# Optimization experiments

Hardware: AMD Instinct MI355X
Metric: run time of the kernel (lower is better)

## Reference

```python
import jax, jax.numpy as jnp
import numpy as np

NHEAD = 8
K_NEIGH = 16


def setup_inputs() -> dict:
    key = jax.random.key(0)
    ks = jax.random.split(key, 6)
    B, L, D = 4, 4096, 512
    x = jax.random.normal(ks[0], (B, L, D), dtype=jnp.float32)
    positions = jax.random.uniform(ks[1], (B, L, 3), dtype=jnp.float32)
    in_proj_w = jax.random.normal(ks[2], (3 * D, D), dtype=jnp.float32) * 0.02
    in_proj_b = jax.random.normal(ks[3], (3 * D,), dtype=jnp.float32) * 0.02
    out_proj_w = jax.random.normal(ks[4], (D, D), dtype=jnp.float32) * 0.02
    out_proj_b = jax.random.normal(ks[5], (D,), dtype=jnp.float32) * 0.02
    return {"x": x, "positions": positions, "in_proj_w": in_proj_w,
            "in_proj_b": in_proj_b, "out_proj_w": out_proj_w, "out_proj_b": out_proj_b}


def _sparse_attention(x, positions, in_proj_w, in_proj_b, out_proj_w, out_proj_b):
    B, L, D = x.shape
    H, dh = NHEAD, D // NHEAD
    K = min(K_NEIGH, L)
    scale = 1.0 / jnp.sqrt(jnp.asarray(dh, x.dtype))

    # Pairwise distances [B, L, L]; topk smallest -> neighbor indices [B, L, K].
    diff = positions[:, :, None, :] - positions[:, None, :, :]
    dist = jnp.sqrt(jnp.sum(diff * diff, axis=-1))
    _, nbr = jax.lax.top_k(-dist, K)  # [B, L, K]

    Wq, Wk, Wv = in_proj_w[:D], in_proj_w[D:2 * D], in_proj_w[2 * D:]
    bq, bk, bv = in_proj_b[:D], in_proj_b[D:2 * D], in_proj_b[2 * D:]

    # Query is x[b, i] itself (self is always its own nearest neighbor at dist 0),
    # so the selected attention row equals attention with query x[b, i] over neighbors.
    q = ((x @ Wq.T + bq) * scale).reshape(B, L, H, dh)

    # Gather neighbor features: [B, L, K, D]
    b_idx = jnp.arange(B)[:, None, None]
    local_x = x[b_idx, nbr]
    k = (local_x @ Wk.T + bk).reshape(B, L, K, H, dh)
    v = (local_x @ Wv.T + bv).reshape(B, L, K, H, dh)

    scores = jnp.einsum('blhd,blkhd->blhk', q, k)
    attn = jax.nn.softmax(scores, axis=-1)
    ctx = jnp.einsum('blhk,blkhd->blhd', attn, v).reshape(B, L, D)
    out = ctx @ out_proj_w.T + out_proj_b

    # Faithful fallback: if i not among its neighbors, pass through x[b, i].
    is_in = jnp.any(nbr == jnp.arange(L)[None, :, None], axis=-1)  # [B, L]
    return jnp.where(is_in[..., None], out, x)


def reference(x, positions, in_proj_w, in_proj_b, out_proj_w, out_proj_b):
    return _sparse_attention(x, positions, in_proj_w, in_proj_b, out_proj_w, out_proj_b)
```

## Files before the change

kernel.cpp:

```cpp
#include <hip/hip_runtime.h>
#include <cfloat>
#include <cmath>

constexpr int B = 4;
constexpr int L = 4096;
constexpr int D = 512;
constexpr int NH = 8;
constexpr int DH = 64;
constexpr int KN = 16;
constexpr int M = B * L;
constexpr int N_IN = 3 * D;
constexpr int NCELL = 512;

typedef __attribute__((ext_vector_type(8))) short short8;
typedef __attribute__((ext_vector_type(4))) float f32x4;
typedef unsigned short ushort;

__device__ __forceinline__ ushort f2bf(float f) {
  unsigned u = __float_as_uint(f);
  u = u + 0x7fffu + ((u >> 16) & 1u);
  return (ushort)(u >> 16);
}
__device__ __forceinline__ float bf2f(ushort h) {
  return __uint_as_float(((unsigned)h) << 16);
}
__device__ __forceinline__ float dot8(const uint4 qu, const uint4 ku, float a) {
  a = fmaf(bf2f((ushort)qu.x), bf2f((ushort)ku.x), a);
  a = fmaf(bf2f((ushort)(qu.x >> 16)), bf2f((ushort)(ku.x >> 16)), a);
  a = fmaf(bf2f((ushort)qu.y), bf2f((ushort)ku.y), a);
  a = fmaf(bf2f((ushort)(qu.y >> 16)), bf2f((ushort)(ku.y >> 16)), a);
  a = fmaf(bf2f((ushort)qu.z), bf2f((ushort)ku.z), a);
  a = fmaf(bf2f((ushort)(qu.z >> 16)), bf2f((ushort)(ku.z >> 16)), a);
  a = fmaf(bf2f((ushort)qu.w), bf2f((ushort)ku.w), a);
  a = fmaf(bf2f((ushort)(qu.w >> 16)), bf2f((ushort)(ku.w >> 16)), a);
  return a;
}
__device__ __forceinline__ void acc8(float wgt, const uint4 vv, float (&acc)[8]) {
  acc[0] = fmaf(wgt, bf2f((ushort)vv.x), acc[0]);
  acc[1] = fmaf(wgt, bf2f((ushort)(vv.x >> 16)), acc[1]);
  acc[2] = fmaf(wgt, bf2f((ushort)vv.y), acc[2]);
  acc[3] = fmaf(wgt, bf2f((ushort)(vv.y >> 16)), acc[3]);
  acc[4] = fmaf(wgt, bf2f((ushort)vv.z), acc[4]);
  acc[5] = fmaf(wgt, bf2f((ushort)(vv.z >> 16)), acc[5]);
  acc[6] = fmaf(wgt, bf2f((ushort)vv.w), acc[6]);
  acc[7] = fmaf(wgt, bf2f((ushort)(vv.w >> 16)), acc[7]);
}
__device__ __forceinline__ uint2 pack4hi(const float4 v) {
  uint2 o;
  o.x = (unsigned)f2bf(v.x) | ((unsigned)f2bf(v.y) << 16);
  o.y = (unsigned)f2bf(v.z) | ((unsigned)f2bf(v.w) << 16);
  return o;
}
__device__ __forceinline__ void gload16(const void* g, void* l) {
  __builtin_amdgcn_global_load_lds(
      (const __attribute__((address_space(1))) void*)g,
      (__attribute__((address_space(3))) void*)l, 16, 0, 0);
}
__device__ __forceinline__ int morton3(int x, int y, int z) {
  int m = 0;
#pragma unroll
  for (int i = 0; i < 3; ++i)
    m |= (((x >> i) & 1) << (3 * i + 2)) | (((y >> i) & 1) << (3 * i + 1)) |
         (((z >> i) & 1) << (3 * i));
  return m;
}

constexpr int SORT_BLKS = B;
constexpr int CVTX_BLKS = 1024;
constexpr int CVTW_BLKS = 256;
constexpr int STAGE0_BLKS = SORT_BLKS + CVTX_BLKS + CVTW_BLKS;

__global__ __launch_bounds__(512) void stage0_kernel(
    const float* __restrict__ pos, const float* __restrict__ x,
    const float* __restrict__ in_w, const float* __restrict__ out_w,
    int* __restrict__ qorder, ushort* __restrict__ xb,
    ushort* __restrict__ iwh, ushort* __restrict__ owh,
    ushort* __restrict__ owl) {
  __shared__ int hist[NCELL];
  __shared__ int scanbuf[NCELL];

  const int bid = blockIdx.x;
  const int tid = threadIdx.x;

  if (bid < SORT_BLKS) {
    const int b = bid;
    const int t = tid;
    hist[t] = 0;
    __syncthreads();

    int cells[8], ranks[8];
    const float* p = pos + (size_t)b * L * 3;
#pragma unroll
    for (int q = 0; q < 8; ++q) {
      const int i = q * 512 + t;
      const int ix = min(7, max(0, (int)(p[3 * i + 0] * 8.f)));
      const int iy = min(7, max(0, (int)(p[3 * i + 1] * 8.f)));
      const int iz = min(7, max(0, (int)(p[3 * i + 2] * 8.f)));
      cells[q] = morton3(ix, iy, iz);
      ranks[q] = atomicAdd(&hist[cells[q]], 1);
    }
    __syncthreads();

    int accv = hist[t];
    const int orig = accv;
    scanbuf[t] = accv;
    __syncthreads();
    for (int s = 1; s < NCELL; s <<= 1) {
      const int o = (t >= s) ? scanbuf[t - s] : 0;
      __syncthreads();
      accv += o;
      scanbuf[t] = accv;
      __syncthreads();
    }
    hist[t] = accv - orig;
    __syncthreads();

#pragma unroll
    for (int q = 0; q < 8; ++q) {
      const int i = q * 512 + t;
      qorder[b * L + hist[cells[q]] + ranks[q]] = i;
    }

  } else if (bid < SORT_BLKS + CVTX_BLKS) {
    const int vb = bid - SORT_BLKS;
    const int n8 = M * D / 8;
    for (int i = vb * 512 + tid; i < n8; i += CVTX_BLKS * 512) {
      const float4 v0 = reinterpret_cast<const float4*>(x)[i * 2];
      const float4 v1 = reinterpret_cast<const float4*>(x)[i * 2 + 1];
      uint4 o;
      const uint2 a = pack4hi(v0), b2 = pack4hi(v1);
      o.x = a.x; o.y = a.y; o.z = b2.x; o.w = b2.y;
      reinterpret_cast<uint4*>(xb)[i] = o;
    }

  } else {
    const int vb = bid - SORT_BLKS - CVTX_BLKS;
    const int ni8 = N_IN * D / 8;
    const int no8 = D * D / 8;
    for (int i = vb * 512 + tid; i < ni8 + no8; i += CVTW_BLKS * 512) {
      if (i < ni8) {
        const float4 v0 = reinterpret_cast<const float4*>(in_w)[i * 2];
        const float4 v1 = reinterpret_cast<const float4*>(in_w)[i * 2 + 1];
        uint4 o;
        const uint2 a = pack4hi(v0), b2 = pack4hi(v1);
        o.x = a.x; o.y = a.y; o.z = b2.x; o.w = b2.y;
        reinterpret_cast<uint4*>(iwh)[i] = o;
      } else {
        const int j = i - ni8;
        const float4 v0 = reinterpret_cast<const float4*>(out_w)[j * 2];
        const float4 v1 = reinterpret_cast<const float4*>(out_w)[j * 2 + 1];
        uint4 oh, ol;
        const uint2 a = pack4hi(v0), b2 = pack4hi(v1);
        oh.x = a.x; oh.y = a.y; oh.z = b2.x; oh.w = b2.y;
        const float4 r0 = make_float4(v0.x - bf2f(f2bf(v0.x)), v0.y - bf2f(f2bf(v0.y)),
                                      v0.z - bf2f(f2bf(v0.z)), v0.w - bf2f(f2bf(v0.w)));
        const float4 r1 = make_float4(v1.x - bf2f(f2bf(v1.x)), v1.y - bf2f(f2bf(v1.y)),
                                      v1.z - bf2f(f2bf(v1.z)), v1.w - bf2f(f2bf(v1.w)));
        const uint2 c = pack4hi(r0), d2 = pack4hi(r1);
        ol.x = c.x; ol.y = c.y; ol.z = d2.x; ol.w = d2.y;
        reinterpret_cast<uint4*>(owh)[j] = oh;
        reinterpret_cast<uint4*>(owl)[j] = ol;
      }
    }
  }
}

constexpr int TP = 65;

__global__ __launch_bounds__(512) void topk_attn_kernel(
    const float* __restrict__ pos, const ushort* __restrict__ qb,
    const ushort* __restrict__ kb, const ushort* __restrict__ vb,
    const int* __restrict__ qorder, int* __restrict__ isin,
    ushort* __restrict__ ctx) {
  __shared__ float sxT[64 * TP], syT[64 * TP], szT[64 * TP];
  __shared__ unsigned long long lst[8 * 64];
  __shared__ int nbw[8][KN];

  const int wave = threadIdx.x >> 6;
  const int lane = threadIdx.x & 63;
  const int xcd = blockIdx.x & 7;
  const int chunk = blockIdx.x >> 3;
  const int b = xcd >> 1;
  const int slot = ((xcd & 1) * 256 + chunk) * 8 + wave;
  const int l = qorder[b * L + slot];
  const int row = b * L + l;
  const int bbase = b * L;

  const float* p = pos + (size_t)b * L * 3;
  for (int i = threadIdx.x; i < L; i += 512) {
    const int a = (i & 63) * TP + (i >> 6);
    sxT[a] = p[3 * i + 0];
    syT[a] = p[3 * i + 1];
    szT[a] = p[3 * i + 2];
  }
  __syncthreads();

  const int qa = (l & 63) * TP + (l >> 6);
  const float qx = sxT[qa], qy = syT[qa], qz = szT[qa];

  float mA = FLT_MAX, mB2 = FLT_MAX, mC = FLT_MAX, mD2 = FLT_MAX;
  const int base = lane * TP;
  for (int j = 0; j < 64; j += 4) {
#define D2(t, acc)                                                   \
    {                                                                \
      const int a = base + j + t;                                    \
      const float dx = qx - sxT[a], dy = qy - syT[a], dz = qz - szT[a]; \
      acc = fminf(acc, fmaf(dx, dx, fmaf(dy, dy, dz * dz)));         \
    }
    D2(0, mA) D2(1, mB2) D2(2, mC) D2(3, mD2)
#undef D2
  }
  const unsigned mbits = __float_as_uint(fminf(fminf(mA, mB2), fminf(mC, mD2)));

  unsigned lo = 1, hi = 0x40400001u;
  while (lo < hi) {
    const unsigned mid = (lo + hi) >> 1;
    const int c = __popcll(__ballot(mbits < mid));
    if (c >= 16) hi = mid; else lo = mid + 1;
  }
  const unsigned P = lo + 16;

  int cnt = 0;
  unsigned long long am = __ballot(mbits < P);
  const unsigned long long below = (1ull << lane) - 1ull;
  while (am) {
    const int pl = (int)__builtin_ctzll(am);
    am &= am - 1;
    const int a = pl * TP + lane;
    const float dx = qx - sxT[a], dy = qy - syT[a], dz = qz - szT[a];
    const float d2 = fmaf(dx, dx, fmaf(dy, dy, dz * dz));
    const bool hit = __float_as_uint(d2) < P;
    const unsigned long long msk = __ballot(hit);
    if (hit) {
      const int slot2 = cnt + __popcll(msk & below);
      if (slot2 < 64) {
        const unsigned c = (unsigned)(lane * 64 + pl);
        lst[wave * 64 + slot2] =
            ((unsigned long long)__float_as_uint(sqrtf(d2)) << 32) | c;
      }
    }
    cnt += __popcll(msk);
  }
  const int n = min(cnt, 64);

  const unsigned long long mine = (lane < n) ? lst[wave * 64 + lane] : ~0ull;
  int r = 0;
  for (int i = 0; i < n; ++i) r += (lst[wave * 64 + i] < mine) ? 1 : 0;

  const int nidx = (int)(unsigned)(mine & 0xffffffffu);
  const bool wr = (lane < n) && (r < 16);
  if (wr) nbw[wave][r] = nidx;
  const unsigned long long hit2 = __ballot(wr && nidx == l);
  if (lane == 0) isin[row] = hit2 ? 1 : 0;

  const int h = lane >> 3;
  const int n0 = lane & 7;
  const int glane = h * 8;

  const ushort* qp = qb + (size_t)row * D + h * DH;
  uint4 qv[8];
#pragma unroll
  for (int i = 0; i < 8; ++i)
    qv[i] = *reinterpret_cast<const uint4*>(qp + i * 8);

  const int j0 = nbw[wave][n0];
  const int j1 = nbw[wave][n0 + 8];
  float a0 = 0.f, a1 = 0.f;
  {
    const ushort* kr0 = kb + (size_t)(bbase + j0) * D + h * DH;
    const ushort* kr1 = kb + (size_t)(bbase + j1) * D + h * DH;
#pragma unroll
    for (int i = 0; i < 8; ++i) {
      a0 = dot8(qv[i], *reinterpret_cast<const uint4*>(kr0 + i * 8), a0);
      a1 = dot8(qv[i], *reinterpret_cast<const uint4*>(kr1 + i * 8), a1);
    }
  }

  float mx = fmaxf(a0, a1);
  mx = fmaxf(mx, __shfl_xor(mx, 1));
  mx = fmaxf(mx, __shfl_xor(mx, 2));
  mx = fmaxf(mx, __shfl_xor(mx, 4));
  const float e0 = expf(a0 - mx), e1 = expf(a1 - mx);
  float sm = e0 + e1;
  sm += __shfl_xor(sm, 1);
  sm += __shfl_xor(sm, 2);
  sm += __shfl_xor(sm, 4);
  const float inv = 1.0f / sm;
  const float w0 = e0 * inv, w1 = e1 * inv;

  float ww[KN];
  int jj[KN];
#pragma unroll
  for (int nn = 0; nn < KN; ++nn) {
    ww[nn] = __shfl((nn < 8) ? w0 : w1, glane + (nn & 7));
    jj[nn] = nbw[wave][nn];
  }

  const int d0 = n0 * 8;
  const ushort* vbase = vb + (size_t)bbase * D + h * DH + d0;
  float acc[8];
#pragma unroll
  for (int i = 0; i < 8; ++i) acc[i] = 0.f;

#pragma unroll
  for (int g = 0; g < KN; g += 4) {
    const uint4 va0 = *reinterpret_cast<const uint4*>(vbase + (size_t)jj[g] * D);
    const uint4 va1 = *reinterpret_cast<const uint4*>(vbase + (size_t)jj[g + 1] * D);
    const uint4 va2 = *reinterpret_cast<const uint4*>(vbase + (size_t)jj[g + 2] * D);
    const uint4 va3 = *reinterpret_cast<const uint4*>(vbase + (size_t)jj[g + 3] * D);
    acc8(ww[g], va0, acc);
    acc8(ww[g + 1], va1, acc);
    acc8(ww[g + 2], va2, acc);
    acc8(ww[g + 3], va3, acc);
  }

  uint4 o;
  o.x = (unsigned)f2bf(acc[0]) | ((unsigned)f2bf(acc[1]) << 16);
  o.y = (unsigned)f2bf(acc[2]) | ((unsigned)f2bf(acc[3]) << 16);
  o.z = (unsigned)f2bf(acc[4]) | ((unsigned)f2bf(acc[5]) << 16);
  o.w = (unsigned)f2bf(acc[6]) | ((unsigned)f2bf(acc[7]) << 16);
  *reinterpret_cast<uint4*>(ctx + (size_t)row * D + h * DH + d0) = o;
}

constexpr int BM = 128, BN = 128;
constexpr int BK2 = 64;

__global__ __launch_bounds__(256) void gemm_in(const ushort* __restrict__ A,
                                               const ushort* __restrict__ W,
                                               const float* __restrict__ bias,
                                               ushort* __restrict__ qb,
                                               ushort* __restrict__ kb,
                                               ushort* __restrict__ vb) {
  __shared__ ushort Ah[BM * BK2];
  __shared__ ushort Bh[BN * BK2];

  const int tid = threadIdx.x;
  const int m0 = blockIdx.x * BM;
  const int n0 = blockIdx.y * BN;

  const int wv = tid >> 6;
  const int lane = tid & 63;
  const int srow0 = wv * 8 + (lane >> 3);
  const int gchunk = (lane & 7) ^ (lane >> 3);
  const ushort* Asrc = A + (size_t)(m0 + srow0) * D + gchunk * 8;
  const ushort* Wsrc = W + (size_t)(n0 + srow0) * D + gchunk * 8;
  ushort* AhB0 = Ah + (wv * 8) * BK2;
  ushort* AhB1 = Ah + (wv * 8 + 32) * BK2;
  ushort* AhB2 = Ah + (wv * 8 + 64) * BK2;
  ushort* AhB3 = Ah + (wv * 8 + 96) * BK2;
  ushort* BhB0 = Bh + (wv * 8) * BK2;
  ushort* BhB1 = Bh + (wv * 8 + 32) * BK2;
  ushort* BhB2 = Bh + (wv * 8 + 64) * BK2;
  ushort* BhB3 = Bh + (wv * 8 + 96) * BK2;

  const int wr0 = (wv >> 1) * 64;
  const int wc0 = (wv & 1) * 64;
  const int fr_row = lane & 15;
  const int cbase = lane >> 4;
  const int rx = lane & 7;

  f32x4 acc[4][4];
#pragma unroll
  for (int i = 0; i < 4; ++i)
#pragma unroll
    for (int j = 0; j < 4; ++j) acc[i][j] = {0.f, 0.f, 0.f, 0.f};

  for (int k0 = 0; k0 < D; k0 += BK2) {
    __syncthreads();
    gload16(Asrc + k0, AhB0);
    gload16(Asrc + (size_t)32 * D + k0, AhB1);
    gload16(Asrc + (size_t)64 * D + k0, AhB2);
    gload16(Asrc + (size_t)96 * D + k0, AhB3);
    gload16(Wsrc + k0, BhB0);
    gload16(Wsrc + (size_t)32 * D + k0, BhB1);
    gload16(Wsrc + (size_t)64 * D + k0, BhB2);
    gload16(Wsrc + (size_t)96 * D + k0, BhB3);
    __syncthreads();

#pragma unroll
    for (int kk = 0; kk < 2; ++kk) {
      const int slot = (kk * 4 + cbase) ^ rx;
      short8 ah[4];
#pragma unroll
      for (int fr = 0; fr < 4; ++fr)
        ah[fr] = *reinterpret_cast<const short8*>(
            &Ah[(wr0 + fr * 16 + fr_row) * BK2 + slot * 8]);
#pragma unroll
      for (int fc = 0; fc < 4; ++fc) {
        const short8 bh = *reinterpret_cast<const short8*>(
            &Bh[(wc0 + fc * 16 + fr_row) * BK2 + slot * 8]);
#pragma unroll
        for (int fr = 0; fr < 4; ++fr)
          acc[fr][fc] = __builtin_amdgcn_mfma_f32_16x16x32_bf16(ah[fr], bh, acc[fr][fc], 0, 0, 0);
      }
    }
  }

  const int region = n0 >> 9;
  ushort* outb = region == 0 ? qb : (region == 1 ? kb : vb);
  const float scl = region == 0 ? 0.125f : 1.0f;
  const int nloc0 = (n0 & 511) + wc0;
#pragma unroll
  for (int fr = 0; fr < 4; ++fr) {
#pragma unroll
    for (int r = 0; r < 4; ++r) {
      const int grow = m0 + wr0 + fr * 16 + (lane >> 4) * 4 + r;
#pragma unroll
      for (int fc = 0; fc < 4; ++fc) {
        const int cc = fc * 16 + (lane & 15);
        const float v = (acc[fr][fc][r] + bias[n0 + wc0 + cc]) * scl;
        outb[(size_t)grow * D + nloc0 + cc] = f2bf(v);
      }
    }
  }
}

__global__ __launch_bounds__(256) void gemm_out(const ushort* __restrict__ A,
                                                const ushort* __restrict__ Wh,
                                                const ushort* __restrict__ Wl,
                                                const float* __restrict__ bias,
                                                float* __restrict__ C,
                                                const float* __restrict__ X,
                                                const int* __restrict__ isin) {
  __shared__ ushort Ah[BM * BK2];
  __shared__ ushort Bh[BN * BK2];
  __shared__ ushort Bl[BN * BK2];

  const int tid = threadIdx.x;
  const int m0 = blockIdx.x * BM;
  const int n0 = blockIdx.y * BN;

  const int wv = tid >> 6;
  const int lane = tid & 63;
  const int srow0 = wv * 8 + (lane >> 3);
  const int gchunk = (lane & 7) ^ (lane >> 3);
  const ushort* Asrc = A + (size_t)(m0 + srow0) * D + gchunk * 8;
  const ushort* Hsrc = Wh + (size_t)(n0 + srow0) * D + gchunk * 8;
  const ushort* Lsrc = Wl + (size_t)(n0 + srow0) * D + gchunk * 8;
  ushort* AhB0 = Ah + (wv * 8) * BK2;
  ushort* AhB1 = Ah + (wv * 8 + 32) * BK2;
  ushort* AhB2 = Ah + (wv * 8 + 64) * BK2;
  ushort* AhB3 = Ah + (wv * 8 + 96) * BK2;
  ushort* BhB0 = Bh + (wv * 8) * BK2;
  ushort* BhB1 = Bh + (wv * 8 + 32) * BK2;
  ushort* BhB2 = Bh + (wv * 8 + 64) * BK2;
  ushort* BhB3 = Bh + (wv * 8 + 96) * BK2;
  ushort* BlB0 = Bl + (wv * 8) * BK2;
  ushort* BlB1 = Bl + (wv * 8 + 32) * BK2;
  ushort* BlB2 = Bl + (wv * 8 + 64) * BK2;
  ushort* BlB3 = Bl + (wv * 8 + 96) * BK2;

  const int wr0 = (wv >> 1) * 64;
  const int wc0 = (wv & 1) * 64;
  const int fr_row = lane & 15;
  const int cbase = lane >> 4;
  const int rx = lane & 7;

  f32x4 acc[4][4];
#pragma unroll
  for (int i = 0; i < 4; ++i)
#pragma unroll
    for (int j = 0; j < 4; ++j) acc[i][j] = {0.f, 0.f, 0.f, 0.f};

  for (int k0 = 0; k0 < D; k0 += BK2) {
    __syncthreads();
    gload16(Asrc + k0, AhB0);
    gload16(Asrc + (size_t)32 * D + k0, AhB1);
    gload16(Asrc + (size_t)64 * D + k0, AhB2);
    gload16(Asrc + (size_t)96 * D + k0, AhB3);
    gload16(Hsrc + k0, BhB0);
    gload16(Hsrc + (size_t)32 * D + k0, BhB1);
    gload16(Hsrc + (size_t)64 * D + k0, BhB2);
    gload16(Hsrc + (size_t)96 * D + k0, BhB3);
    gload16(Lsrc + k0, BlB0);
    gload16(Lsrc + (size_t)32 * D + k0, BlB1);
    gload16(Lsrc + (size_t)64 * D + k0, BlB2);
    gload16(Lsrc + (size_t)96 * D + k0, BlB3);
    __syncthreads();

#pragma unroll
    for (int kk = 0; kk < 2; ++kk) {
      const int slot = (kk * 4 + cbase) ^ rx;
      short8 ah[4];
#pragma unroll
      for (int fr = 0; fr < 4; ++fr)
        ah[fr] = *reinterpret_cast<const short8*>(
            &Ah[(wr0 + fr * 16 + fr_row) * BK2 + slot * 8]);
#pragma unroll
      for (int fc = 0; fc < 4; ++fc) {
        const short8 bh = *reinterpret_cast<const short8*>(
            &Bh[(wc0 + fc * 16 + fr_row) * BK2 + slot * 8]);
        const short8 bl = *reinterpret_cast<const short8*>(
            &Bl[(wc0 + fc * 16 + fr_row) * BK2 + slot * 8]);
#pragma unroll
        for (int fr = 0; fr < 4; ++fr) {
          acc[fr][fc] = __builtin_amdgcn_mfma_f32_16x16x32_bf16(ah[fr], bh, acc[fr][fc], 0, 0, 0);
          acc[fr][fc] = __builtin_amdgcn_mfma_f32_16x16x32_bf16(ah[fr], bl, acc[fr][fc], 0, 0, 0);
        }
      }
    }
  }

#pragma unroll
  for (int fr = 0; fr < 4; ++fr) {
#pragma unroll
    for (int r = 0; r < 4; ++r) {
      const int grow = m0 + wr0 + fr * 16 + (lane >> 4) * 4 + r;
      const int ok = isin[grow];
#pragma unroll
      for (int fc = 0; fc < 4; ++fc) {
        const int gcol = n0 + wc0 + fc * 16 + (lane & 15);
        float v = acc[fr][fc][r] + bias[gcol];
        if (!ok) v = X[(size_t)grow * D + gcol];
        C[(size_t)grow * D + gcol] = v;
      }
    }
  }
}

extern "C" void kernel_launch(void* const* d_in, const int* in_sizes, int n_in,
                              void* d_out, int out_size, void* d_ws, size_t ws_size,
                              hipStream_t stream) {
  const float* x     = (const float*)d_in[0];
  const float* pos   = (const float*)d_in[1];
  const float* in_w  = (const float*)d_in[2];
  const float* in_b  = (const float*)d_in[3];
  const float* out_w = (const float*)d_in[4];
  const float* out_b = (const float*)d_in[5];
  float* out = (float*)d_out;

  const size_t isin_bytes = (size_t)M * sizeof(int);
  const size_t half_bytes = (size_t)M * D * sizeof(ushort);
  const size_t iwh_bytes  = (size_t)N_IN * D * sizeof(ushort);
  const size_t ow_bytes   = (size_t)D * D * sizeof(ushort);
  const size_t sort_bytes = (size_t)M * sizeof(int);
  const size_t need = isin_bytes + 5 * half_bytes +
                      iwh_bytes + 2 * ow_bytes + sort_bytes + 16384;
  if (ws_size < need) return;

  char* w = (char*)d_ws;
  int*    isin   = (int*)w;    w += (isin_bytes + 255) & ~(size_t)255;
  ushort* xb     = (ushort*)w; w += (half_bytes + 255) & ~(size_t)255;
  ushort* qb     = (ushort*)w; w += (half_bytes + 255) & ~(size_t)255;
  ushort* kb     = (ushort*)w; w += (half_bytes + 255) & ~(size_t)255;
  ushort* vb     = (ushort*)w; w += (half_bytes + 255) & ~(size_t)255;
  ushort* ctxb   = (ushort*)w; w += (half_bytes + 255) & ~(size_t)255;
  ushort* iwh    = (ushort*)w; w += (iwh_bytes + 255) & ~(size_t)255;
  ushort* owh    = (ushort*)w; w += (ow_bytes + 255) & ~(size_t)255;
  ushort* owl    = (ushort*)w; w += (ow_bytes + 255) & ~(size_t)255;
  int*    qorder = (int*)w;

  stage0_kernel<<<STAGE0_BLKS, 512, 0, stream>>>(
      pos, x, in_w, out_w, qorder, xb, iwh, owh, owl);

  gemm_in<<<dim3(M / BM, N_IN / BN), 256, 0, stream>>>(xb, iwh, in_b, qb, kb, vb);

  topk_attn_kernel<<<M / 8, 512, 0, stream>>>(pos, qb, kb, vb, qorder, isin, ctxb);

  gemm_out<<<dim3(M / BM, D / BN), 256, 0, stream>>>(ctxb, owh, owl, out_b, out, x, isin);
}
```

Baseline: 151.6 us.

## Replace brute-force kNN scan with 3x3x3 uniform-grid cell search plus fallback

The stage0 sort now writes cell-sorted positions (packed as float4 with the original index) plus per-cell offsets and counts. The top-k kernel then scans only the 27 neighbouring cells instead of staging all 4096 batch positions in shared memory and scanning them per query. A correctness check on the neighbour count and the 16th distance triggers a full brute-force fallback when the local search may be incomplete. This removes the per-block shared-memory load of all positions and the O(L) distance work, at the cost of shared atomics, divergent per-cell loops and an occasional slow path.

```diff
diff --git a/kernel.cpp b/kernel.cpp
--- a/kernel.cpp
+++ b/kernel.cpp
@@ -15,6 +15,7 @@
 typedef __attribute__((ext_vector_type(8))) short short8;
 typedef __attribute__((ext_vector_type(4))) float f32x4;
 typedef unsigned short ushort;
+typedef unsigned long long ull;
 
 __device__ __forceinline__ ushort f2bf(float f) {
   unsigned u = __float_as_uint(f);
@@ -73,9 +74,9 @@
 __global__ __launch_bounds__(512) void stage0_kernel(
     const float* __restrict__ pos, const float* __restrict__ x,
     const float* __restrict__ in_w, const float* __restrict__ out_w,
-    int* __restrict__ qorder, ushort* __restrict__ xb,
-    ushort* __restrict__ iwh, ushort* __restrict__ owh,
-    ushort* __restrict__ owl) {
+    float4* __restrict__ ps, int* __restrict__ offsG, int* __restrict__ cntG,
+    ushort* __restrict__ xb, ushort* __restrict__ iwh,
+    ushort* __restrict__ owh, ushort* __restrict__ owl) {
   __shared__ int hist[NCELL];
   __shared__ int scanbuf[NCELL];
 
@@ -115,10 +116,15 @@
     hist[t] = accv - orig;
     __syncthreads();
 
+    offsG[b * NCELL + t] = hist[t];
+    cntG[b * NCELL + t] = orig;
+
 #pragma unroll
     for (int q = 0; q < 8; ++q) {
       const int i = q * 512 + t;
-      qorder[b * L + hist[cells[q]] + ranks[q]] = i;
+      const int slot = hist[cells[q]] + ranks[q];
+      ps[b * L + slot] = make_float4(p[3 * i + 0], p[3 * i + 1], p[3 * i + 2],
+                                     __int_as_float(i));
     }
 
   } else if (bid < SORT_BLKS + CVTX_BLKS) {
@@ -165,16 +171,14 @@
   }
 }
 
-constexpr int TP = 65;
-
 __global__ __launch_bounds__(512) void topk_attn_kernel(
-    const float* __restrict__ pos, const ushort* __restrict__ qb,
+    const float4* __restrict__ ps, const int* __restrict__ offsG,
+    const int* __restrict__ cntG, const ushort* __restrict__ qb,
     const ushort* __restrict__ kb, const ushort* __restrict__ vb,
-    const int* __restrict__ qorder, int* __restrict__ isin,
-    ushort* __restrict__ ctx) {
-  __shared__ float sxT[64 * TP], syT[64 * TP], szT[64 * TP];
-  __shared__ unsigned long long lst[8 * 64];
+    int* __restrict__ isin, ushort* __restrict__ ctx) {
+  __shared__ ull lst[8 * 64];
   __shared__ int nbw[8][KN];
+  __shared__ int cntW[8];
 
   const int wave = threadIdx.x >> 6;
   const int lane = threadIdx.x & 63;
@@ -182,36 +186,47 @@
   const int chunk = blockIdx.x >> 3;
   const int b = xcd >> 1;
   const int slot = ((xcd & 1) * 256 + chunk) * 8 + wave;
-  const int l = qorder[b * L + slot];
-  const int row = b * L + l;
   const int bbase = b * L;
 
-  const float* p = pos + (size_t)b * L * 3;
-  for (int i = threadIdx.x; i < L; i += 512) {
-    const int a = (i & 63) * TP + (i >> 6);
-    sxT[a] = p[3 * i + 0];
-    syT[a] = p[3 * i + 1];
-    szT[a] = p[3 * i + 2];
-  }
-  __syncthreads();
-
-  const int qa = (l & 63) * TP + (l >> 6);
-  const float qx = sxT[qa], qy = syT[qa], qz = szT[qa];
-
-  float mA = FLT_MAX, mB2 = FLT_MAX, mC = FLT_MAX, mD2 = FLT_MAX;
-  const int base = lane * TP;
-  for (int j = 0; j < 64; j += 4) {
-#define D2(t, acc)                                                   \
-    {                                                                \
-      const int a = base + j + t;                                    \
-      const float dx = qx - sxT[a], dy = qy - syT[a], dz = qz - szT[a]; \
-      acc = fminf(acc, fmaf(dx, dx, fmaf(dy, dy, dz * dz)));         \
-    }
-    D2(0, mA) D2(1, mB2) D2(2, mC) D2(3, mD2)
-#undef D2
-  }
-  const unsigned mbits = __float_as_uint(fminf(fminf(mA, mB2), fminf(mC, mD2)));
-
+  const float4 qp4 = ps[bbase + slot];
+  const int l = __float_as_int(qp4.w);
+  const int row = bbase + l;
+
+  const int ix = min(7, max(0, (int)(qp4.x * 8.f)));
+  const int iy = min(7, max(0, (int)(qp4.y * 8.f)));
+  const int iz = min(7, max(0, (int)(qp4.z * 8.f)));
+
+  if (lane == 0) cntW[wave] = 0;
+
+  const int g = lane >> 3;
+  const int li = lane & 7;
+  float md2 = FLT_MAX;
+  int tot_part = 0;
+#pragma unroll
+  for (int u = 0; u < 4; ++u) {
+    const int t = g + 8 * u;
+    if (t < 27) {
+      const int cx = ix + (t % 3) - 1;
+      const int cy = iy + ((t / 3) % 3) - 1;
+      const int cz = iz + (t / 9) - 1;
+      if (cx >= 0 && cx < 8 && cy >= 0 && cy < 8 && cz >= 0 && cz < 8) {
+        const int cid = morton3(cx, cy, cz);
+        const int off = offsG[b * NCELL + cid];
+        const int cn = cntG[b * NCELL + cid];
+        if (li == 0) tot_part += cn;
+        for (int s2 = li; s2 < cn; s2 += 8) {
+          const float4 c4 = ps[bbase + off + s2];
+          const float ddx = qp4.x - c4.x, ddy = qp4.y - c4.y, ddz = qp4.z - c4.z;
+          md2 = fminf(md2, fmaf(ddx, ddx, fmaf(ddy, ddy, ddz * ddz)));
+        }
+      }
+    }
+  }
+  int tot = tot_part;
+#pragma unroll
+  for (int s = 1; s < 64; s <<= 1) tot += __shfl_xor(tot, s, 64);
+
+  const unsigned mbits = __float_as_uint(md2);
   unsigned lo = 1, hi = 0x40400001u;
   while (lo < hi) {
     const unsigned mid = (lo + hi) >> 1;
@@ -220,38 +235,88 @@
   }
   const unsigned P = lo + 16;
 
-  int cnt = 0;
-  unsigned long long am = __ballot(mbits < P);
-  const unsigned long long below = (1ull << lane) - 1ull;
-  while (am) {
-    const int pl = (int)__builtin_ctzll(am);
-    am &= am - 1;
-    const int a = pl * TP + lane;
-    const float dx = qx - sxT[a], dy = qy - syT[a], dz = qz - szT[a];
-    const float d2 = fmaf(dx, dx, fmaf(dy, dy, dz * dz));
-    const bool hit = __float_as_uint(d2) < P;
-    const unsigned long long msk = __ballot(hit);
-    if (hit) {
-      const int slot2 = cnt + __popcll(msk & below);
-      if (slot2 < 64) {
-        const unsigned c = (unsigned)(lane * 64 + pl);
-        lst[wave * 64 + slot2] =
-            ((unsigned long long)__float_as_uint(sqrtf(d2)) << 32) | c;
-      }
-    }
-    cnt += __popcll(msk);
-  }
-  const int n = min(cnt, 64);
-
-  const unsigned long long mine = (lane < n) ? lst[wave * 64 + lane] : ~0ull;
+#pragma unroll
+  for (int u = 0; u < 4; ++u) {
+    const int t = g + 8 * u;
+    if (t < 27) {
+      const int cx = ix + (t % 3) - 1;
+      const int cy = iy + ((t / 3) % 3) - 1;
+      const int cz = iz + (t / 9) - 1;
+      if (cx >= 0 && cx < 8 && cy >= 0 && cy < 8 && cz >= 0 && cz < 8) {
+        const int cid = morton3(cx, cy, cz);
+        const int off = offsG[b * NCELL + cid];
+        const int cn = cntG[b * NCELL + cid];
+        for (int s2 = li; s2 < cn; s2 += 8) {
+          const float4 c4 = ps[bbase + off + s2];
+          const float ddx = qp4.x - c4.x, ddy = qp4.y - c4.y, ddz = qp4.z - c4.z;
+          const float d2v = fmaf(ddx, ddx, fmaf(ddy, ddy, ddz * ddz));
+          if (__float_as_uint(d2v) < P) {
+            const int sl = atomicAdd(&cntW[wave], 1);
+            if (sl < 64)
+              lst[wave * 64 + sl] = ((ull)__float_as_uint(sqrtf(d2v)) << 32) |
+                                    (unsigned)__float_as_int(c4.w);
+          }
+        }
+      }
+    }
+  }
+  int n = min(cntW[wave], 64);
+
+  ull mine = (lane < n) ? lst[wave * 64 + lane] : ~0ull;
   int r = 0;
   for (int i = 0; i < n; ++i) r += (lst[wave * 64 + i] < mine) ? 1 : 0;
-
-  const int nidx = (int)(unsigned)(mine & 0xffffffffu);
-  const bool wr = (lane < n) && (r < 16);
+  int nidx = (int)(unsigned)(mine & 0xffffffffu);
+  bool wr = (lane < n) && (r < 16);
   if (wr) nbw[wave][r] = nidx;
-  const unsigned long long hit2 = __ballot(wr && nidx == l);
+  ull hit2 = __ballot(wr && nidx == l);
   if (lane == 0) isin[row] = hit2 ? 1 : 0;
+
+  unsigned sb = wr ? (unsigned)(mine >> 32) : 0u;
+#pragma unroll
+  for (int s = 1; s < 64; s <<= 1) sb = max(sb, (unsigned)__shfl_xor(sb, s, 64));
+  const bool okfast = (tot >= 16) && (__uint_as_float(sb) < 0.125f);
+
+  if (!okfast) {
+    float fm = FLT_MAX;
+    for (int c = 0; c < 64; ++c) {
+      const float4 c4 = ps[bbase + c * 64 + lane];
+      const float ddx = qp4.x - c4.x, ddy = qp4.y - c4.y, ddz = qp4.z - c4.z;
+      fm = fminf(fm, fmaf(ddx, ddx, fmaf(ddy, ddy, ddz * ddz)));
+    }
+    const unsigned fb = __float_as_uint(fm);
+    unsigned lo2 = 1, hi2 = 0x40400001u;
+    while (lo2 < hi2) {
+      const unsigned mid = (lo2 + hi2) >> 1;
+      const int c = __popcll(__ballot(fb < mid));
+      if (c >= 16) hi2 = mid; else lo2 = mid + 1;
+    }
+    const unsigned P2 = lo2 + 16;
+    const ull below = (1ull << lane) - 1ull;
+    int cnt2 = 0;
+    for (int c = 0; c < 64; ++c) {
+      const float4 c4 = ps[bbase + c * 64 + lane];
+      const float ddx = qp4.x - c4.x, ddy = qp4.y - c4.y, ddz = qp4.z - c4.z;
+      const float d2v = fmaf(ddx, ddx, fmaf(ddy, ddy, ddz * ddz));
+      const bool hit = __float_as_uint(d2v) < P2;
+      const ull msk = __ballot(hit);
+      if (hit) {
+        const int sl = cnt2 + __popcll(msk & below);
+        if (sl < 64)
+          lst[wave * 64 + sl] = ((ull)__float_as_uint(sqrtf(d2v)) << 32) |
+                                (unsigned)__float_as_int(c4.w);
+      }
+      cnt2 += __popcll(msk);
+    }
+    n = min(cnt2, 64);
+    mine = (lane < n) ? lst[wave * 64 + lane] : ~0ull;
+    r = 0;
+    for (int i = 0; i < n; ++i) r += (lst[wave * 64 + i] < mine) ? 1 : 0;
+    nidx = (int)(unsigned)(mine & 0xffffffffu);
+    wr = (lane < n) && (r < 16);
+    if (wr) nbw[wave][r] = nidx;
+    hit2 = __ballot(wr && nidx == l);
+    if (lane == 0) isin[row] = hit2 ? 1 : 0;
+  }
 
   const int h = lane >> 3;
   const int n0 = lane & 7;
@@ -303,15 +368,15 @@
   for (int i = 0; i < 8; ++i) acc[i] = 0.f;
 
 #pragma unroll
-  for (int g = 0; g < KN; g += 4) {
-    const uint4 va0 = *reinterpret_cast<const uint4*>(vbase + (size_t)jj[g] * D);
-    const uint4 va1 = *reinterpret_cast<const uint4*>(vbase + (size_t)jj[g + 1] * D);
-    const uint4 va2 = *reinterpret_cast<const uint4*>(vbase + (size_t)jj[g + 2] * D);
-    const uint4 va3 = *reinterpret_cast<const uint4*>(vbase + (size_t)jj[g + 3] * D);
-    acc8(ww[g], va0, acc);
-    acc8(ww[g + 1], va1, acc);
-    acc8(ww[g + 2], va2, acc);
-    acc8(ww[g + 3], va3, acc);
+  for (int gI = 0; gI < KN; gI += 4) {
+    const uint4 va0 = *reinterpret_cast<const uint4*>(vbase + (size_t)jj[gI] * D);
+    const uint4 va1 = *reinterpret_cast<const uint4*>(vbase + (size_t)jj[gI + 1] * D);
+    const uint4 va2 = *reinterpret_cast<const uint4*>(vbase + (size_t)jj[gI + 2] * D);
+    const uint4 va3 = *reinterpret_cast<const uint4*>(vbase + (size_t)jj[gI + 3] * D);
+    acc8(ww[gI], va0, acc);
+    acc8(ww[gI + 1], va1, acc);
+    acc8(ww[gI + 2], va2, acc);
+    acc8(ww[gI + 3], va3, acc);
   }
 
   uint4 o;
@@ -533,9 +598,10 @@
   const size_t half_bytes = (size_t)M * D * sizeof(ushort);
   const size_t iwh_bytes  = (size_t)N_IN * D * sizeof(ushort);
   const size_t ow_bytes   = (size_t)D * D * sizeof(ushort);
-  const size_t sort_bytes = (size_t)M * sizeof(int);
-  const size_t need = isin_bytes + 5 * half_bytes +
-                      iwh_bytes + 2 * ow_bytes + sort_bytes + 16384;
+  const size_t ps_bytes   = (size_t)M * sizeof(float4);
+  const size_t cell_bytes = (size_t)B * NCELL * sizeof(int);
+  const size_t need = isin_bytes + 5 * half_bytes + iwh_bytes +
+                      2 * ow_bytes + ps_bytes + 2 * cell_bytes + 16384;
   if (ws_size < need) return;
 
   char* w = (char*)d_ws;
@@ -548,14 +614,17 @@
   ushort* iwh    = (ushort*)w; w += (iwh_bytes + 255) & ~(size_t)255;
   ushort* owh    = (ushort*)w; w += (ow_bytes + 255) & ~(size_t)255;
   ushort* owl    = (ushort*)w; w += (ow_bytes + 255) & ~(size_t)255;
-  int*    qorder = (int*)w;
+  float4* ps     = (float4*)w; w += (ps_bytes + 255) & ~(size_t)255;
+  int*    offsG  = (int*)w;    w += (cell_bytes + 255) & ~(size_t)255;
+  int*    cntG   = (int*)w;
 
   stage0_kernel<<<STAGE0_BLKS, 512, 0, stream>>>(
-      pos, x, in_w, out_w, qorder, xb, iwh, owh, owl);
+      pos, x, in_w, out_w, ps, offsG, cntG, xb, iwh, owh, owl);
 
   gemm_in<<<dim3(M / BM, N_IN / BN), 256, 0, stream>>>(xb, iwh, in_b, qb, kb, vb);
 
-  topk_attn_kernel<<<M / 8, 512, 0, stream>>>(pos, qb, kb, vb, qorder, isin, ctxb);
+  topk_attn_kernel<<<M / 8, 512, 0, stream>>>(ps, offsG, cntG, qb, kb, vb,
+                                              isin, ctxb);
 
   gemm_out<<<dim3(M / BM, D / BN), 256, 0, stream>>>(ctxb, owh, owl, out_b, out, x, isin);
 }
```

After: 169.3 us. 1.12x slower.
